# Kernel tuning notes

Measured on AMD Instinct MI355X. Metric: run time of the kernel, lower is better.

## Reference

```python
import jax, jax.numpy as jnp
import numpy as np

B, T, D_MODEL, D_INT = 8, 2048, 1024, 128
ROPE_BASE = 10000.0


def setup_inputs() -> dict:
    key = jax.random.key(0)
    k1, k2 = jax.random.split(key)
    x = jax.random.normal(k1, (B, T, D_MODEL), dtype=jnp.float32)
    # Linear(d_model, 3*d_internal, bias=False): weight [3*d_int, d_model]
    W_qkv = jax.random.normal(k2, (3 * D_INT, D_MODEL), dtype=jnp.float32) * (D_MODEL ** -0.5)
    sqk = (D_MODEL ** -0.5) * jnp.ones((D_INT,), dtype=jnp.float32)
    return {"x": x, "W_qkv": W_qkv, "sqk": sqk}


def _rotate_half(u):
    u1, u2 = jnp.split(u, 2, axis=-1)
    return jnp.concatenate([-u2, u1], axis=-1)


def reference(x, W_qkv, sqk):
    Bq, Tq, C = x.shape
    d = W_qkv.shape[0] // 3
    # fused QKV projection
    qkv = jnp.einsum('btc,dc->btd', x, W_qkv)  # [B,T,3d]
    q, k, v = jnp.split(qkv, 3, axis=-1)       # each [B,T,d]
    # rotary embeddings over full head dim
    inv_freq = 1.0 / (ROPE_BASE ** (jnp.arange(0, d, 2, dtype=jnp.float32) / d))
    t = jnp.arange(Tq, dtype=jnp.float32)
    freqs = t[:, None] * inv_freq[None, :]       # [T, d/2]
    emb = jnp.concatenate([freqs, freqs], -1)     # [T, d]
    cos, sin = jnp.cos(emb), jnp.sin(emb)
    q = q * cos + _rotate_half(q) * sin
    k = k * cos + _rotate_half(k) * sin
    # L2-normalize then scale by sqk (nGPT-style)
    q = q / jnp.linalg.norm(q, axis=-1, keepdims=True) * sqk
    k = k / jnp.linalg.norm(k, axis=-1, keepdims=True) * sqk
    # causal SDPA with scale = sqrt(d_model) (multiplier, as in the source)
    scale = jnp.asarray(C, jnp.float32) ** 0.5
    scores = jnp.einsum('bqd,bkd->bqk', q, k) * scale  # [B,T,T]
    causal = jnp.tril(jnp.ones((Tq, Tq), dtype=bool))
    scores = jnp.where(causal, scores, jnp.finfo(scores.dtype).min)
    attn = jax.nn.softmax(scores, axis=-1)
    out = jnp.einsum('bqk,bkd->bqd', attn, v)  # [B,T,d]
    return out
```

## Files before the change

### kernel.cpp

```cpp
#include <hip/hip_runtime.h>
#include <math.h>

#define BB 8
#define TT 2048
#define DM 1024
#define DH 128
#define US unsigned short

typedef short s8v __attribute__((ext_vector_type(8)));
typedef US us8 __attribute__((ext_vector_type(8)));
typedef float f4v __attribute__((ext_vector_type(4)));

__device__ __forceinline__ US f2bf(float f) {
  uint u = __float_as_uint(f);
  uint r = (u + 0x7fffu + ((u >> 16) & 1u)) >> 16;
  return (US)r;
}
__device__ __forceinline__ float bf2f(US h) {
  return __uint_as_float(((uint)h) << 16);
}
__device__ __forceinline__ void cvt4(const float4 v, uint2& h, uint2& lo) {
  US h0 = f2bf(v.x), h1 = f2bf(v.y), h2 = f2bf(v.z), h3 = f2bf(v.w);
  US l0 = f2bf(v.x - bf2f(h0)), l1 = f2bf(v.y - bf2f(h1)),
     l2 = f2bf(v.z - bf2f(h2)), l3 = f2bf(v.w - bf2f(h3));
  h = make_uint2((uint)h0 | ((uint)h1 << 16), (uint)h2 | ((uint)h3 << 16));
  lo = make_uint2((uint)l0 | ((uint)l1 << 16), (uint)l2 | ((uint)l3 << 16));
}

#define XHI 0
#define XLO 2048
#define WHI 4096
#define WLO 16384
#define NEG_L2B_64 -0.20762050593549395f

__global__ __launch_bounds__(512) void qkv_rope_norm(
    const float* __restrict__ x, const float* __restrict__ W,
    const float* __restrict__ sqk, US* __restrict__ qbf, US* __restrict__ kbf,
    US* __restrict__ vhT, US* __restrict__ vlT) {
  __shared__ __align__(16) US smem_u[28672];
  const int tid = threadIdx.x;
  const int m0 = blockIdx.x * 64;

  const int srow = tid >> 3;
  const int c4 = tid & 7;
  const int k8s = c4 >> 1, half = c4 & 1;
  const float* xg = x + (size_t)(m0 + srow) * DM + (c4 << 2);
  const float* wg = W + (size_t)srow * DM + (c4 << 2);
  const int xeo = (k8s * 64 + srow) * 8 + half * 4;

  const int l = tid & 63, w = tid >> 6;
  const int wm = w >> 2, wn = w & 3;
  const int lr = l & 15, k8l = l >> 4;
  const int arow = wm * 32;

  f4v acc[2][6];
#pragma unroll
  for (int r = 0; r < 2; ++r)
#pragma unroll
    for (int c = 0; c < 6; ++c) acc[r][c] = (f4v)(0.f);

  float4 gx = *(const float4*)(xg);
  float4 gw[6];
#pragma unroll
  for (int i = 0; i < 6; ++i) gw[i] = *(const float4*)(wg + (size_t)i * 64 * DM);

  for (int kc = 0; kc < 32; ++kc) {
    __syncthreads();
    {
      uint2 h, lo;
      cvt4(gx, h, lo);
      *(uint2*)&smem_u[XHI + xeo] = h;
      *(uint2*)&smem_u[XLO + xeo] = lo;
#pragma unroll
      for (int i = 0; i < 6; ++i) {
        int weo = (k8s * 384 + srow + 64 * i) * 8 + half * 4;
        cvt4(gw[i], h, lo);
        *(uint2*)&smem_u[WHI + weo] = h;
        *(uint2*)&smem_u[WLO + weo] = lo;
      }
    }
    {
      int kn = (kc < 31) ? (kc + 1) * 32 : 0;
      gx = *(const float4*)(xg + kn);
#pragma unroll
      for (int i = 0; i < 6; ++i)
        gw[i] = *(const float4*)(wg + (size_t)i * 64 * DM + kn);
    }
    __syncthreads();
    s8v axh[2], axl[2];
#pragma unroll
    for (int r = 0; r < 2; ++r) {
      int ao = (k8l * 64 + arow + r * 16 + lr) * 8;
      axh[r] = *(const s8v*)&smem_u[XHI + ao];
      axl[r] = *(const s8v*)&smem_u[XLO + ao];
    }
#pragma unroll
    for (int c = 0; c < 6; ++c) {
      int bo = (k8l * 384 + wn * 96 + c * 16 + lr) * 8;
      s8v bh = *(const s8v*)&smem_u[WHI + bo];
      s8v bl = *(const s8v*)&smem_u[WLO + bo];
#pragma unroll
      for (int r = 0; r < 2; ++r) {
        acc[r][c] =
            __builtin_amdgcn_mfma_f32_16x16x32_bf16(axh[r], bh, acc[r][c], 0, 0, 0);
        acc[r][c] =
            __builtin_amdgcn_mfma_f32_16x16x32_bf16(axl[r], bh, acc[r][c], 0, 0, 0);
        acc[r][c] =
            __builtin_amdgcn_mfma_f32_16x16x32_bf16(axh[r], bl, acc[r][c], 0, 0, 0);
      }
    }
  }

  __syncthreads();
  float* buf = (float*)smem_u;
  const int prow = tid >> 3, sub = tid & 7;
  const int q4row = (l >> 4) * 4;
  const int bq = m0 >> 11;
  const int t0 = m0 & (TT - 1);
  const float t_pos = (float)(t0 + prow);

#pragma unroll
  for (int p = 0; p < 3; ++p) {
#pragma unroll
    for (int c = 0; c < 6; ++c) {
      int nbase = wn * 96 + c * 16;
      if ((nbase >> 7) == p) {
        int coloff = nbase & 127;
#pragma unroll
        for (int r = 0; r < 2; ++r)
#pragma unroll
          for (int q = 0; q < 4; ++q)
            buf[(arow + r * 16 + q4row + q) * 132 + coloff + lr] = acc[r][c][q];
      }
    }
    __syncthreads();
    if (p == 2) {
      const int dv = tid >> 2;
      const int rr = (tid & 3) * 16;
      us8 h0, h1, l0, l1;
#pragma unroll
      for (int i = 0; i < 8; ++i) {
        float va = buf[(rr + i) * 132 + dv];
        float vb2 = buf[(rr + 8 + i) * 132 + dv];
        US ha = f2bf(va), hb = f2bf(vb2);
        h0[i] = ha; h1[i] = hb;
        l0[i] = f2bf(va - bf2f(ha));
        l1[i] = f2bf(vb2 - bf2f(hb));
      }
      size_t base = ((size_t)bq * DH + dv) * TT + t0 + rr;
      *(us8*)(vhT + base) = h0;
      *(us8*)(vhT + base + 8) = h1;
      *(us8*)(vlT + base) = l0;
      *(us8*)(vlT + base + 8) = l1;
    } else {
      const float* br = &buf[prow * 132 + sub * 16];
      float4 a0 = *(const float4*)(br + 0);
      float4 a1 = *(const float4*)(br + 4);
      float4 a2 = *(const float4*)(br + 8);
      float4 a3 = *(const float4*)(br + 12);
      float vals[16] = {a0.x, a0.y, a0.z, a0.w, a1.x, a1.y, a1.z, a1.w,
                        a2.x, a2.y, a2.z, a2.w, a3.x, a3.y, a3.z, a3.w};
      float ov[16];
      float ss = 0.f;
#pragma unroll
      for (int j = 0; j < 16; ++j) {
        float val = vals[j];
        float partner = __shfl_xor(val, 4);
        int fi = ((sub & 3) * 16) + j;
        float ang = t_pos * exp2f((float)fi * NEG_L2B_64);
        float sn, cs;
        sincosf(ang, &sn, &cs);
        float rot = (sub < 4) ? -partner : partner;
        float o = fmaf(val, cs, rot * sn);
        ov[j] = o;
        ss = fmaf(o, o, ss);
      }
      ss += __shfl_xor(ss, 1);
      ss += __shfl_xor(ss, 2);
      ss += __shfl_xor(ss, 4);
      float rn = 1.0f / sqrtf(ss);
      const float* sqp = sqk + sub * 16;
      US* dst = (p == 0 ? qbf : kbf) + (size_t)(m0 + prow) * DH + sub * 16;
      us8 o0, o1;
#pragma unroll
      for (int j = 0; j < 8; ++j) {
        o0[j] = f2bf(ov[j] * rn * sqp[j]);
        o1[j] = f2bf(ov[8 + j] * rn * sqp[8 + j]);
      }
      *(us8*)dst = o0;
      *(us8*)(dst + 8) = o1;
    }
    __syncthreads();
  }
}

#define BQ 64
#define BK 64
#define SCALE 32.0f
#define NLOC 80
#define NJOB (NLOC * BB)
#define QSO 0
#define KSO 8192
#define VHO 16384
#define VLO 24576
#define PHO 32768
#define PLO 41472
#define SMEM_US 50176

__device__ __forceinline__ int slot_base(int qt) {
  if (qt < 8) return qt;
  if (qt < 16) return 8 + 2 * (qt - 8);
  if (qt < 24) return 24 + 3 * (qt - 16);
  return 48 + 4 * (qt - 24);
}

__global__ __launch_bounds__(256) void attn_causal(
    const US* __restrict__ qbf, const US* __restrict__ kbf,
    const US* __restrict__ vhT, const US* __restrict__ vlT,
    float* __restrict__ pO, float* __restrict__ pm, float* __restrict__ pl) {
  extern __shared__ US sm[];
  const int tid = threadIdx.x;
  const int bi = blockIdx.x;
  const int b = bi & 7;
  const int local = bi >> 3;
  int qt, s;
  if (local < 32) {
    qt = 31 - (local >> 2); s = local & 3;
  } else if (local < 56) {
    int l2 = local - 32; qt = 23 - l2 / 3; s = l2 - (l2 / 3) * 3;
  } else if (local < 72) {
    int l2 = local - 56; qt = 15 - (l2 >> 1); s = l2 & 1;
  } else {
    qt = 7 - (local - 72); s = 0;
  }
  const int S = 1 + (qt >> 3);
  const int nk = qt + 1;
  const int kt0 = (s * nk) / S;
  const int kt1 = ((s + 1) * nk) / S;
  const int slot = b * NLOC + slot_base(qt) + s;

  const int ln = tid & 63, w = tid >> 6;
  const int wrow = w * 16;
  const int l15 = ln & 15, l4 = ln >> 4;

  {
    const int d8 = tid & 15, r0 = tid >> 4;
    const US* src = qbf + ((size_t)b * TT + (size_t)qt * BQ) * DH + d8 * 8;
#pragma unroll
    for (int p = 0; p < 4; ++p) {
      int r = r0 + p * 16;
      us8 v = *(const us8*)(src + (size_t)r * DH);
      *(us8*)&sm[QSO + (d8 * 64 + (r ^ (d8 & 7))) * 8] = v;
    }
  }

  float m[4], lsum[4];
  f4v o[8];
#pragma unroll
  for (int q = 0; q < 4; ++q) { m[q] = -1e30f; lsum[q] = 0.f; }
#pragma unroll
  for (int c8 = 0; c8 < 8; ++c8) o[c8] = (f4v)(0.f);

  for (int kt = kt0; kt < kt1; ++kt) {
    __syncthreads();
    {
      const int d8 = tid & 15, r0 = tid >> 4;
      const US* src = kbf + ((size_t)b * TT + (size_t)kt * BK) * DH + d8 * 8;
#pragma unroll
      for (int p = 0; p < 4; ++p) {
        int r = r0 + p * 16;
        us8 v = *(const us8*)(src + (size_t)r * DH);
        *(us8*)&sm[KSO + (d8 * 64 + (r ^ (d8 & 7))) * 8] = v;
      }
    }
    {
      const int kv8 = tid & 7, dv0 = tid >> 3;
      const size_t gb = (size_t)b * DH * TT + (size_t)kt * BK + kv8 * 8;
#pragma unroll
      for (int p = 0; p < 4; ++p) {
        int dv = dv0 + p * 32;
        us8 vh = *(const us8*)(vhT + gb + (size_t)dv * TT);
        us8 vl = *(const us8*)(vlT + gb + (size_t)dv * TT);
        *(us8*)&sm[VHO + (kv8 * 128 + dv) * 8] = vh;
        *(us8*)&sm[VLO + (kv8 * 128 + dv) * 8] = vl;
      }
    }
    __syncthreads();

    f4v sfr[4];
#pragma unroll
    for (int c = 0; c < 4; ++c) sfr[c] = (f4v)(0.f);
#pragma unroll
    for (int ks = 0; ks < 4; ++ks) {
      const int d8 = ks * 4 + l4;
      const int perm = (l15 ^ (d8 & 7));
      s8v a = *(const s8v*)&sm[QSO + (d8 * 64 + wrow + perm) * 8];
#pragma unroll
      for (int c = 0; c < 4; ++c) {
        s8v bk = *(const s8v*)&sm[KSO + (d8 * 64 + c * 16 + perm) * 8];
        sfr[c] = __builtin_amdgcn_mfma_f32_16x16x32_bf16(a, bk, sfr[c], 0, 0, 0);
      }
    }

    const bool diag = (kt == qt);
    float alpha[4];
#pragma unroll
    for (int q = 0; q < 4; ++q) {
      const int rowg = qt * BQ + wrow + l4 * 4 + q;
      float st[4];
      float mx = -1e30f;
#pragma unroll
      for (int c = 0; c < 4; ++c) {
        float sv = sfr[c][q] * SCALE;
        if (diag && (kt * BK + c * 16 + l15 > rowg)) sv = -1e30f;
        st[c] = sv;
        mx = fmaxf(mx, sv);
      }
      mx = fmaxf(mx, __shfl_xor(mx, 1));
      mx = fmaxf(mx, __shfl_xor(mx, 2));
      mx = fmaxf(mx, __shfl_xor(mx, 4));
      mx = fmaxf(mx, __shfl_xor(mx, 8));
      float mn = fmaxf(m[q], mx);
      float a = __expf(m[q] - mn);
      float rs = 0.f;
      const int prow_off = (wrow + l4 * 4 + q) * 136 + l15;
#pragma unroll
      for (int c = 0; c < 4; ++c) {
        float pv = __expf(st[c] - mn);
        rs += pv;
        US ph = f2bf(pv);
        sm[PHO + prow_off + c * 16] = ph;
        sm[PLO + prow_off + c * 16] = f2bf(pv - bf2f(ph));
      }
      rs += __shfl_xor(rs, 1);
      rs += __shfl_xor(rs, 2);
      rs += __shfl_xor(rs, 4);
      rs += __shfl_xor(rs, 8);
      lsum[q] = lsum[q] * a + rs;
      m[q] = mn;
      alpha[q] = a;
    }

#pragma unroll
    for (int c8 = 0; c8 < 8; ++c8)
#pragma unroll
      for (int q = 0; q < 4; ++q) o[c8][q] *= alpha[q];

#pragma unroll
    for (int ks = 0; ks < 2; ++ks) {
      const int aoff = (wrow + l15) * 136 + ks * 32 + l4 * 8;
      s8v pa = *(const s8v*)&sm[PHO + aoff];
      s8v pb = *(const s8v*)&sm[PLO + aoff];
      const int kv8 = ks * 4 + l4;
#pragma unroll
      for (int c8 = 0; c8 < 8; ++c8) {
        const int vo = (kv8 * 128 + c8 * 16 + l15) * 8;
        s8v vh = *(const s8v*)&sm[VHO + vo];
        s8v vl = *(const s8v*)&sm[VLO + vo];
        o[c8] = __builtin_amdgcn_mfma_f32_16x16x32_bf16(pa, vh, o[c8], 0, 0, 0);
        o[c8] = __builtin_amdgcn_mfma_f32_16x16x32_bf16(pb, vh, o[c8], 0, 0, 0);
        o[c8] = __builtin_amdgcn_mfma_f32_16x16x32_bf16(pa, vl, o[c8], 0, 0, 0);
      }
    }
  }

  float* ob = pO + (size_t)slot * (BQ * DH);
#pragma unroll
  for (int q = 0; q < 4; ++q) {
    const int r = wrow + l4 * 4 + q;
#pragma unroll
    for (int c8 = 0; c8 < 8; ++c8)
      ob[(size_t)r * DH + c8 * 16 + l15] = o[c8][q];
  }
  if (l15 == 0) {
#pragma unroll
    for (int q = 0; q < 4; ++q) {
      pm[slot * BQ + wrow + l4 * 4 + q] = m[q];
      pl[slot * BQ + wrow + l4 * 4 + q] = lsum[q];
    }
  }
}

__global__ __launch_bounds__(256) void attn_merge(
    const float* __restrict__ pO, const float* __restrict__ pm,
    const float* __restrict__ pl, float* __restrict__ out) {
  const int g4 = blockIdx.x * 256 + threadIdx.x;
  const int row = g4 >> 5;
  const int c4 = g4 & 31;
  const int t = row & (TT - 1);
  const int qt = t >> 6;
  const int rloc = t & 63;
  const int b = row >> 11;
  const int S = 1 + (qt >> 3);
  const int base = b * NLOC + slot_base(qt);

  float ms[4], ls[4];
  float mstar = -1e30f;
#pragma unroll
  for (int s = 0; s < 4; ++s) {
    if (s < S) {
      ms[s] = pm[(base + s) * BQ + rloc];
      ls[s] = pl[(base + s) * BQ + rloc];
      mstar = fmaxf(mstar, ms[s]);
    }
  }
  float4 acc = make_float4(0.f, 0.f, 0.f, 0.f);
  float L = 0.f;
#pragma unroll
  for (int s = 0; s < 4; ++s) {
    if (s < S) {
      float wgt = __expf(ms[s] - mstar);
      L += wgt * ls[s];
      float4 o4 = *(const float4*)(pO + (size_t)(base + s) * (BQ * DH) +
                                   (size_t)rloc * DH + (c4 << 2));
      acc.x = fmaf(wgt, o4.x, acc.x);
      acc.y = fmaf(wgt, o4.y, acc.y);
      acc.z = fmaf(wgt, o4.z, acc.z);
      acc.w = fmaf(wgt, o4.w, acc.w);
    }
  }
  float inv = 1.0f / L;
  *(float4*)(out + (size_t)row * DH + (c4 << 2)) =
      make_float4(acc.x * inv, acc.y * inv, acc.z * inv, acc.w * inv);
}

extern "C" void kernel_launch(void* const* d_in, const int* in_sizes, int n_in,
                              void* d_out, int out_size, void* d_ws, size_t ws_size,
                              hipStream_t stream) {
  const float* x = (const float*)d_in[0];
  const float* W = (const float*)d_in[1];
  const float* sqk = (const float*)d_in[2];
  float* out = (float*)d_out;

  const size_t per = (size_t)BB * TT * DH;
  US* qbf = (US*)d_ws;
  US* kbf = qbf + per;
  US* vhT = kbf + per;
  US* vlT = vhT + per;
  float* pO = (float*)(vlT + per);
  float* pm = pO + (size_t)NJOB * BQ * DH;
  float* pl = pm + (size_t)NJOB * BQ;

  qkv_rope_norm<<<dim3(256), dim3(512), 0, stream>>>(x, W, sqk, qbf, kbf,
                                                     vhT, vlT);

  attn_causal<<<dim3(NJOB), dim3(256), SMEM_US * 2, stream>>>(
      qbf, kbf, vhT, vlT, pO, pm, pl);

  attn_merge<<<dim3((BB * TT * DH / 4) / 256), dim3(256), 0, stream>>>(
      pO, pm, pl, out);
}
```

Baseline: 236.8 us.

## Halve key tile to 32, keep Q fragments in registers, shrink LDS

Drops the key/value tile size from 64 to 32 rows and loads each wave's Q fragments straight into registers instead of staging Q in shared memory. LDS per block falls from about 98KB to about 38KB of static arrays, which should allow more blocks per CU and better latency hiding. In exchange the block runs twice as many key iterations, each with its own two barriers and less MFMA work to amortise the load and softmax overhead, and Q now takes more registers. The causal mask condition and iteration counts are adjusted for the half-size tiles.

```diff
diff --git a/kernel.cpp b/kernel.cpp
--- a/kernel.cpp
+++ b/kernel.cpp
@@ -195,17 +195,10 @@
 }
 
 #define BQ 64
-#define BK 64
+#define BK 32
 #define SCALE 32.0f
 #define NLOC 80
 #define NJOB (NLOC * BB)
-#define QSO 0
-#define KSO 8192
-#define VHO 16384
-#define VLO 24576
-#define PHO 32768
-#define PLO 41472
-#define SMEM_US 50176
 
 __device__ __forceinline__ int slot_base(int qt) {
   if (qt < 8) return qt;
@@ -218,7 +211,12 @@
     const US* __restrict__ qbf, const US* __restrict__ kbf,
     const US* __restrict__ vhT, const US* __restrict__ vlT,
     float* __restrict__ pO, float* __restrict__ pm, float* __restrict__ pl) {
-  extern __shared__ US sm[];
+  __shared__ __align__(16) US sK[4096];
+  __shared__ __align__(16) US sVh[4096];
+  __shared__ __align__(16) US sVl[4096];
+  __shared__ __align__(16) US sPh[2560];
+  __shared__ __align__(16) US sPl[2560];
+
   const int tid = threadIdx.x;
   const int bi = blockIdx.x;
   const int b = bi & 7;
@@ -234,7 +232,7 @@
     qt = 7 - (local - 72); s = 0;
   }
   const int S = 1 + (qt >> 3);
-  const int nk = qt + 1;
+  const int nk = 2 * qt + 2;
   const int kt0 = (s * nk) / S;
   const int kt1 = ((s + 1) * nk) / S;
   const int slot = b * NLOC + slot_base(qt) + s;
@@ -243,15 +241,12 @@
   const int wrow = w * 16;
   const int l15 = ln & 15, l4 = ln >> 4;
 
+  s8v qf[4];
   {
-    const int d8 = tid & 15, r0 = tid >> 4;
-    const US* src = qbf + ((size_t)b * TT + (size_t)qt * BQ) * DH + d8 * 8;
-#pragma unroll
-    for (int p = 0; p < 4; ++p) {
-      int r = r0 + p * 16;
-      us8 v = *(const us8*)(src + (size_t)r * DH);
-      *(us8*)&sm[QSO + (d8 * 64 + (r ^ (d8 & 7))) * 8] = v;
-    }
+    const US* qsrc =
+        qbf + ((size_t)b * TT + (size_t)qt * BQ + wrow + l15) * DH + l4 * 8;
+#pragma unroll
+    for (int ks = 0; ks < 4; ++ks) qf[ks] = *(const s8v*)(qsrc + ks * 32);
   }
 
   float m[4], lsum[4];
@@ -267,50 +262,49 @@
       const int d8 = tid & 15, r0 = tid >> 4;
       const US* src = kbf + ((size_t)b * TT + (size_t)kt * BK) * DH + d8 * 8;
 #pragma unroll
-      for (int p = 0; p < 4; ++p) {
+      for (int p = 0; p < 2; ++p) {
         int r = r0 + p * 16;
         us8 v = *(const us8*)(src + (size_t)r * DH);
-        *(us8*)&sm[KSO + (d8 * 64 + (r ^ (d8 & 7))) * 8] = v;
+        *(us8*)&sK[(d8 * 32 + (r ^ (d8 & 7))) * 8] = v;
       }
     }
     {
-      const int kv8 = tid & 7, dv0 = tid >> 3;
+      const int kv8 = tid & 3, dv0 = tid >> 2;
       const size_t gb = (size_t)b * DH * TT + (size_t)kt * BK + kv8 * 8;
 #pragma unroll
-      for (int p = 0; p < 4; ++p) {
-        int dv = dv0 + p * 32;
+      for (int p = 0; p < 2; ++p) {
+        int dv = dv0 + p * 64;
         us8 vh = *(const us8*)(vhT + gb + (size_t)dv * TT);
         us8 vl = *(const us8*)(vlT + gb + (size_t)dv * TT);
-        *(us8*)&sm[VHO + (kv8 * 128 + dv) * 8] = vh;
-        *(us8*)&sm[VLO + (kv8 * 128 + dv) * 8] = vl;
-      }
-    }
-    __syncthreads();
-
-    f4v sfr[4];
-#pragma unroll
-    for (int c = 0; c < 4; ++c) sfr[c] = (f4v)(0.f);
+        *(us8*)&sVh[(kv8 * 128 + dv) * 8] = vh;
+        *(us8*)&sVl[(kv8 * 128 + dv) * 8] = vl;
+      }
+    }
+    __syncthreads();
+
+    f4v sfr[2];
+#pragma unroll
+    for (int c = 0; c < 2; ++c) sfr[c] = (f4v)(0.f);
 #pragma unroll
     for (int ks = 0; ks < 4; ++ks) {
       const int d8 = ks * 4 + l4;
       const int perm = (l15 ^ (d8 & 7));
-      s8v a = *(const s8v*)&sm[QSO + (d8 * 64 + wrow + perm) * 8];
-#pragma unroll
-      for (int c = 0; c < 4; ++c) {
-        s8v bk = *(const s8v*)&sm[KSO + (d8 * 64 + c * 16 + perm) * 8];
-        sfr[c] = __builtin_amdgcn_mfma_f32_16x16x32_bf16(a, bk, sfr[c], 0, 0, 0);
-      }
-    }
-
-    const bool diag = (kt == qt);
+      const int perm2 = ((16 + l15) ^ (d8 & 7));
+      s8v bk0 = *(const s8v*)&sK[(d8 * 32 + perm) * 8];
+      s8v bk1 = *(const s8v*)&sK[(d8 * 32 + perm2) * 8];
+      sfr[0] = __builtin_amdgcn_mfma_f32_16x16x32_bf16(qf[ks], bk0, sfr[0], 0, 0, 0);
+      sfr[1] = __builtin_amdgcn_mfma_f32_16x16x32_bf16(qf[ks], bk1, sfr[1], 0, 0, 0);
+    }
+
+    const bool diag = (kt >= 2 * qt);
     float alpha[4];
 #pragma unroll
     for (int q = 0; q < 4; ++q) {
       const int rowg = qt * BQ + wrow + l4 * 4 + q;
-      float st[4];
+      float st[2];
       float mx = -1e30f;
 #pragma unroll
-      for (int c = 0; c < 4; ++c) {
+      for (int c = 0; c < 2; ++c) {
         float sv = sfr[c][q] * SCALE;
         if (diag && (kt * BK + c * 16 + l15 > rowg)) sv = -1e30f;
         st[c] = sv;
@@ -323,14 +317,14 @@
       float mn = fmaxf(m[q], mx);
       float a = __expf(m[q] - mn);
       float rs = 0.f;
-      const int prow_off = (wrow + l4 * 4 + q) * 136 + l15;
-#pragma unroll
-      for (int c = 0; c < 4; ++c) {
+      const int prow_off = (wrow + l4 * 4 + q) * 40 + l15;
+#pragma unroll
+      for (int c = 0; c < 2; ++c) {
         float pv = __expf(st[c] - mn);
         rs += pv;
         US ph = f2bf(pv);
-        sm[PHO + prow_off + c * 16] = ph;
-        sm[PLO + prow_off + c * 16] = f2bf(pv - bf2f(ph));
+        sPh[prow_off + c * 16] = ph;
+        sPl[prow_off + c * 16] = f2bf(pv - bf2f(ph));
       }
       rs += __shfl_xor(rs, 1);
       rs += __shfl_xor(rs, 2);
@@ -346,17 +340,15 @@
 #pragma unroll
       for (int q = 0; q < 4; ++q) o[c8][q] *= alpha[q];
 
-#pragma unroll
-    for (int ks = 0; ks < 2; ++ks) {
-      const int aoff = (wrow + l15) * 136 + ks * 32 + l4 * 8;
-      s8v pa = *(const s8v*)&sm[PHO + aoff];
-      s8v pb = *(const s8v*)&sm[PLO + aoff];
-      const int kv8 = ks * 4 + l4;
+    {
+      const int aoff = (wrow + l15) * 40 + l4 * 8;
+      s8v pa = *(const s8v*)&sPh[aoff];
+      s8v pb = *(const s8v*)&sPl[aoff];
 #pragma unroll
       for (int c8 = 0; c8 < 8; ++c8) {
-        const int vo = (kv8 * 128 + c8 * 16 + l15) * 8;
-        s8v vh = *(const s8v*)&sm[VHO + vo];
-        s8v vl = *(const s8v*)&sm[VLO + vo];
+        const int vo = (l4 * 128 + c8 * 16 + l15) * 8;
+        s8v vh = *(const s8v*)&sVh[vo];
+        s8v vl = *(const s8v*)&sVl[vo];
         o[c8] = __builtin_amdgcn_mfma_f32_16x16x32_bf16(pa, vh, o[c8], 0, 0, 0);
         o[c8] = __builtin_amdgcn_mfma_f32_16x16x32_bf16(pb, vh, o[c8], 0, 0, 0);
         o[c8] = __builtin_amdgcn_mfma_f32_16x16x32_bf16(pa, vl, o[c8], 0, 0, 0);
@@ -399,8 +391,8 @@
 #pragma unroll
   for (int s = 0; s < 4; ++s) {
     if (s < S) {
-      ms[s] = pm[(base + s) * BQ + rloc];
-      ls[s] = pl[(base + s) * BQ + rloc];
+      ms[s] = pm[(base + s) * 64 + rloc];
+      ls[s] = pl[(base + s) * 64 + rloc];
       mstar = fmaxf(mstar, ms[s]);
     }
   }
@@ -411,7 +403,7 @@
     if (s < S) {
       float wgt = __expf(ms[s] - mstar);
       L += wgt * ls[s];
-      float4 o4 = *(const float4*)(pO + (size_t)(base + s) * (BQ * DH) +
+      float4 o4 = *(const float4*)(pO + (size_t)(base + s) * (64 * DH) +
                                    (size_t)rloc * DH + (c4 << 2));
       acc.x = fmaf(wgt, o4.x, acc.x);
       acc.y = fmaf(wgt, o4.y, acc.y);
@@ -438,14 +430,14 @@
   US* vhT = kbf + per;
   US* vlT = vhT + per;
   float* pO = (float*)(vlT + per);
-  float* pm = pO + (size_t)NJOB * BQ * DH;
-  float* pl = pm + (size_t)NJOB * BQ;
+  float* pm = pO + (size_t)NJOB * 64 * DH;
+  float* pl = pm + (size_t)NJOB * 64;
 
   qkv_rope_norm<<<dim3(256), dim3(512), 0, stream>>>(x, W, sqk, qbf, kbf,
                                                      vhT, vlT);
 
-  attn_causal<<<dim3(NJOB), dim3(256), SMEM_US * 2, stream>>>(
-      qbf, kbf, vhT, vlT, pO, pm, pl);
+  attn_causal<<<dim3(NJOB), dim3(256), 0, stream>>>(qbf, kbf, vhT, vlT, pO,
+                                                    pm, pl);
 
   attn_merge<<<dim3((BB * TT * DH / 4) / 256), dim3(256), 0, stream>>>(
       pO, pm, pl, out);
```

Measured after the change: 215.2 us. 9.1% less time.
